# Kernel optimization log

Measured on AMD Instinct MI355X. Metric: run time of the kernel, lower is better.

Reference implementation:

```python
import jax, jax.numpy as jnp
import numpy as np

N_NODES = 50000
N_SCHEMES = 5
K = 16
HIDDEN = 128
N_CLASSES = 8


def setup_inputs() -> dict:
    key = jax.random.key(0)
    ks = jax.random.split(key, 8)
    sc_nei = jax.random.randint(ks[0], (N_SCHEMES, N_NODES, K), 0, N_NODES)
    feats = jax.random.normal(ks[1], (N_NODES, HIDDEN), dtype=jnp.float32)
    W1 = jax.random.normal(ks[2], (HIDDEN, HIDDEN), dtype=jnp.float32) * (1.0 / np.sqrt(HIDDEN))
    b1 = jnp.zeros((HIDDEN,), dtype=jnp.float32)
    W2 = jax.random.normal(ks[3], (HIDDEN, N_CLASSES), dtype=jnp.float32) * (1.0 / np.sqrt(HIDDEN))
    b2 = jnp.zeros((N_CLASSES,), dtype=jnp.float32)
    alpha = jax.random.normal(ks[4], (N_NODES, 1), dtype=jnp.float32)
    attention = jax.random.normal(ks[5], (N_NODES, N_SCHEMES, 1), dtype=jnp.float32)
    return {"sc_nei": sc_nei, "feats": feats, "W1": W1, "b1": b1,
            "W2": W2, "b2": b2, "alpha": alpha, "attention": attention}


def _mlp(x, W1, b1, W2, b2):
    # MLP2 with num_layers=2, dropout in eval mode (identity)
    h = jax.nn.relu(x @ W1 + b1)
    return h @ W2 + b2


def reference(sc_nei, feats, W1, b1, W2, b2, alpha, attention):
    # Per-scheme: gather -> MLP -> exp(log_softmax)=softmax -> mean over neighbors
    emb = feats[sc_nei]                      # [5, N, K, H]
    probs = jax.nn.softmax(_mlp(emb, W1, b1, W2, b2), axis=-1)  # [5, N, K, C]
    sc_cls = probs.mean(axis=2)              # [5, N, C]
    x = jnp.moveaxis(sc_cls, 0, -1)          # [N, C, 5]
    att = jax.nn.softmax(attention, axis=1)  # [N, 5, 1]
    scheme_pred = jnp.squeeze(x @ att, -1)   # [N, C]
    self_pred = jax.nn.softmax(_mlp(feats[:N_NODES], W1, b1, W2, b2), axis=-1)  # [N, C]
    gate = jax.nn.sigmoid(alpha)             # sigmoid(-a) = 1 - sigmoid(a)
    return gate * self_pred + (1.0 - gate) * scheme_pred
```

## Files before the change

### kernel.cpp

```cpp
#include <hip/hip_runtime.h>
#include <math.h>

#define HIDDEN   128
#define NCLS     8
#define NSCHEMES 5
#define KNEI     16

#define MT  64
#define KC  32
#define AS  132
#define WS  136

__global__ __launch_bounds__(256) void mlp_probs(
    const float* __restrict__ feats, const float* __restrict__ W1,
    const float* __restrict__ b1, const float* __restrict__ W2,
    const float* __restrict__ b2, float* __restrict__ probs, int N)
{
    __shared__ float Alds[MT * AS];
    __shared__ float Wc[KC * WS];
    __shared__ float W2lds[HIDDEN * NCLS];
    __shared__ float b1lds[HIDDEN];
    __shared__ float b2lds[NCLS];

    const int tid = threadIdx.x;
    const int nodeBase = blockIdx.x * MT;

    {
        float4 v = ((const float4*)W2)[tid];
        *(float4*)&W2lds[4 * tid] = v;
    }
    if (tid < HIDDEN) b1lds[tid] = b1[tid];
    if (tid < NCLS)   b2lds[tid] = b2[tid];

    #pragma unroll
    for (int idx = tid; idx < MT * HIDDEN / 4; idx += 256) {
        int r = idx >> 5, c4 = idx & 31;
        int n = nodeBase + r; if (n >= N) n = N - 1;
        float4 v = ((const float4*)(feats + (size_t)n * HIDDEN))[c4];
        *(float4*)&Alds[r * AS + 4 * c4] = v;
    }
    __syncthreads();

    const int n0 = tid & 15;
    const int j0 = tid >> 4;

    float acc[4][8];
    #pragma unroll
    for (int r = 0; r < 4; ++r)
        #pragma unroll
        for (int j = 0; j < 8; ++j) acc[r][j] = 0.f;

    for (int kc = 0; kc < HIDDEN; kc += KC) {
        #pragma unroll
        for (int idx = tid; idx < KC * HIDDEN / 4; idx += 256) {
            int i = idx >> 5, c4 = idx & 31;
            float4 v = ((const float4*)(W1 + (size_t)(kc + i) * HIDDEN))[c4];
            *(float4*)&Wc[i * WS + 4 * c4] = v;
        }
        __syncthreads();

        #pragma unroll
        for (int k = 0; k < KC; k += 4) {
            float4 a[4];
            #pragma unroll
            for (int r = 0; r < 4; ++r)
                a[r] = *(const float4*)&Alds[(n0 + 16 * r) * AS + kc + k];
            float4 w[4][2];
            #pragma unroll
            for (int kk = 0; kk < 4; ++kk) {
                w[kk][0] = *(const float4*)&Wc[(k + kk) * WS + 8 * j0];
                w[kk][1] = *(const float4*)&Wc[(k + kk) * WS + 8 * j0 + 4];
            }
            #pragma unroll
            for (int r = 0; r < 4; ++r) {
                float av[4] = {a[r].x, a[r].y, a[r].z, a[r].w};
                #pragma unroll
                for (int kk = 0; kk < 4; ++kk) {
                    acc[r][0] = fmaf(av[kk], w[kk][0].x, acc[r][0]);
                    acc[r][1] = fmaf(av[kk], w[kk][0].y, acc[r][1]);
                    acc[r][2] = fmaf(av[kk], w[kk][0].z, acc[r][2]);
                    acc[r][3] = fmaf(av[kk], w[kk][0].w, acc[r][3]);
                    acc[r][4] = fmaf(av[kk], w[kk][1].x, acc[r][4]);
                    acc[r][5] = fmaf(av[kk], w[kk][1].y, acc[r][5]);
                    acc[r][6] = fmaf(av[kk], w[kk][1].z, acc[r][6]);
                    acc[r][7] = fmaf(av[kk], w[kk][1].w, acc[r][7]);
                }
            }
        }
        __syncthreads();
    }

    #pragma unroll
    for (int r = 0; r < 4; ++r) {
        int row = n0 + 16 * r;
        float4 h0, h1;
        h0.x = fmaxf(acc[r][0] + b1lds[8 * j0 + 0], 0.f);
        h0.y = fmaxf(acc[r][1] + b1lds[8 * j0 + 1], 0.f);
        h0.z = fmaxf(acc[r][2] + b1lds[8 * j0 + 2], 0.f);
        h0.w = fmaxf(acc[r][3] + b1lds[8 * j0 + 3], 0.f);
        h1.x = fmaxf(acc[r][4] + b1lds[8 * j0 + 4], 0.f);
        h1.y = fmaxf(acc[r][5] + b1lds[8 * j0 + 5], 0.f);
        h1.z = fmaxf(acc[r][6] + b1lds[8 * j0 + 6], 0.f);
        h1.w = fmaxf(acc[r][7] + b1lds[8 * j0 + 7], 0.f);
        *(float4*)&Alds[row * AS + 8 * j0]     = h0;
        *(float4*)&Alds[row * AS + 8 * j0 + 4] = h1;
    }
    __syncthreads();

    float (*Opart)[MT][9] = (float (*)[MT][9])Wc;
    {
        const int node = tid & 63;
        const int jr   = tid >> 6;
        float o[NCLS];
        #pragma unroll
        for (int c = 0; c < NCLS; ++c) o[c] = 0.f;
        #pragma unroll
        for (int jj = 0; jj < 32; jj += 4) {
            int j = jr * 32 + jj;
            float4 h = *(const float4*)&Alds[node * AS + j];
            float hv[4] = {h.x, h.y, h.z, h.w};
            #pragma unroll
            for (int q = 0; q < 4; ++q) {
                float4 w0 = *(const float4*)&W2lds[(j + q) * NCLS];
                float4 w1 = *(const float4*)&W2lds[(j + q) * NCLS + 4];
                o[0] = fmaf(hv[q], w0.x, o[0]);
                o[1] = fmaf(hv[q], w0.y, o[1]);
                o[2] = fmaf(hv[q], w0.z, o[2]);
                o[3] = fmaf(hv[q], w0.w, o[3]);
                o[4] = fmaf(hv[q], w1.x, o[4]);
                o[5] = fmaf(hv[q], w1.y, o[5]);
                o[6] = fmaf(hv[q], w1.z, o[6]);
                o[7] = fmaf(hv[q], w1.w, o[7]);
            }
        }
        #pragma unroll
        for (int c = 0; c < NCLS; ++c) Opart[jr][node][c] = o[c];
    }
    __syncthreads();

    if (tid < MT) {
        int n = nodeBase + tid;
        if (n < N) {
            float o[NCLS];
            #pragma unroll
            for (int c = 0; c < NCLS; ++c)
                o[c] = b2lds[c] + Opart[0][tid][c] + Opart[1][tid][c]
                     + Opart[2][tid][c] + Opart[3][tid][c];
            float m = o[0];
            #pragma unroll
            for (int c = 1; c < NCLS; ++c) m = fmaxf(m, o[c]);
            float s = 0.f;
            #pragma unroll
            for (int c = 0; c < NCLS; ++c) { o[c] = __expf(o[c] - m); s += o[c]; }
            float inv = 1.f / s;
            float4* op = (float4*)(probs + (size_t)n * NCLS);
            op[0] = make_float4(o[0] * inv, o[1] * inv, o[2] * inv, o[3] * inv);
            op[1] = make_float4(o[4] * inv, o[5] * inv, o[6] * inv, o[7] * inv);
        }
    }
}

__global__ __launch_bounds__(256) void combine(
    const int* __restrict__ nei, const float* __restrict__ probs,
    const float* __restrict__ attention, const float* __restrict__ alpha,
    float* __restrict__ out, int N)
{
    int t = blockIdx.x * 256 + threadIdx.x;
    int n = t >> 3;
    int c = t & 7;
    if (n >= N) return;

    float aw[NSCHEMES];
    float m = -1e30f;
    #pragma unroll
    for (int s = 0; s < NSCHEMES; ++s) {
        aw[s] = attention[(size_t)n * NSCHEMES + s];
        m = fmaxf(m, aw[s]);
    }
    float ssum = 0.f;
    #pragma unroll
    for (int s = 0; s < NSCHEMES; ++s) { aw[s] = __expf(aw[s] - m); ssum += aw[s]; }
    float invs = 1.f / ssum;

    float acc = 0.f;
    #pragma unroll
    for (int s = 0; s < NSCHEMES; ++s) {
        const int* ip = nei + ((size_t)s * N + n) * KNEI;
        int4 q0 = ((const int4*)ip)[0];
        int4 q1 = ((const int4*)ip)[1];
        int4 q2 = ((const int4*)ip)[2];
        int4 q3 = ((const int4*)ip)[3];
        float p[KNEI];
        p[ 0] = probs[(size_t)q0.x * NCLS + c];
        p[ 1] = probs[(size_t)q0.y * NCLS + c];
        p[ 2] = probs[(size_t)q0.z * NCLS + c];
        p[ 3] = probs[(size_t)q0.w * NCLS + c];
        p[ 4] = probs[(size_t)q1.x * NCLS + c];
        p[ 5] = probs[(size_t)q1.y * NCLS + c];
        p[ 6] = probs[(size_t)q1.z * NCLS + c];
        p[ 7] = probs[(size_t)q1.w * NCLS + c];
        p[ 8] = probs[(size_t)q2.x * NCLS + c];
        p[ 9] = probs[(size_t)q2.y * NCLS + c];
        p[10] = probs[(size_t)q2.z * NCLS + c];
        p[11] = probs[(size_t)q2.w * NCLS + c];
        p[12] = probs[(size_t)q3.x * NCLS + c];
        p[13] = probs[(size_t)q3.y * NCLS + c];
        p[14] = probs[(size_t)q3.z * NCLS + c];
        p[15] = probs[(size_t)q3.w * NCLS + c];
        float sum = ((p[0] + p[1]) + (p[2] + p[3])) + ((p[4] + p[5]) + (p[6] + p[7]))
                  + ((p[8] + p[9]) + (p[10] + p[11])) + ((p[12] + p[13]) + (p[14] + p[15]));
        acc = fmaf(aw[s] * invs * (1.f / (float)KNEI), sum, acc);
    }

    float g = 1.f / (1.f + __expf(-alpha[n]));
    float self = probs[(size_t)n * NCLS + c];
    out[t] = g * self + (1.f - g) * acc;
}

extern "C" void kernel_launch(void* const* d_in, const int* in_sizes, int n_in,
                              void* d_out, int out_size, void* d_ws, size_t ws_size,
                              hipStream_t stream) {
    const int*   sc_nei    = (const int*)d_in[0];
    const float* feats     = (const float*)d_in[1];
    const float* W1        = (const float*)d_in[2];
    const float* b1        = (const float*)d_in[3];
    const float* W2        = (const float*)d_in[4];
    const float* b2        = (const float*)d_in[5];
    const float* alpha     = (const float*)d_in[6];
    const float* attention = (const float*)d_in[7];
    float* out = (float*)d_out;

    int N = in_sizes[1] / HIDDEN;

    float* probs = (float*)d_ws;

    mlp_probs<<<(N + MT - 1) / MT, 256, 0, stream>>>(feats, W1, b1, W2, b2, probs, N);
    combine<<<((N * NCLS) + 255) / 256, 256, 0, stream>>>(sc_nei, probs, attention, alpha, out, N);
}
```

Baseline: 144.9 us.

## Stream feature chunks into small LDS tile and fuse second layer in registers

The full 64x128 feature tile in LDS is replaced by a 64x32 chunk reloaded for each K-chunk. This cuts LDS use per block so more blocks can be resident. The second linear layer is now computed straight from the first-layer accumulators in registers, with partial class sums reduced by cross-lane shuffles and a small LDS reduction across waves. This removes the hidden-activation LDS write/read and a barrier, but adds per-chunk feature loads, extra register pressure from the o[4][8] array, and shuffles.

```diff
diff --git a/kernel.cpp b/kernel.cpp
--- a/kernel.cpp
+++ b/kernel.cpp
@@ -6,43 +6,33 @@
 #define NSCHEMES 5
 #define KNEI     16
 
-#define MT  64
-#define KC  32
-#define AS  132
-#define WS  136
+#define MT   64
+#define KC   32
+#define ASTR 36
+#define WSTR 136
 
 __global__ __launch_bounds__(256) void mlp_probs(
     const float* __restrict__ feats, const float* __restrict__ W1,
     const float* __restrict__ b1, const float* __restrict__ W2,
     const float* __restrict__ b2, float* __restrict__ probs, int N)
 {
-    __shared__ float Alds[MT * AS];
-    __shared__ float Wc[KC * WS];
+    __shared__ float Ach[MT * ASTR];
+    __shared__ float Wc[KC * WSTR];
     __shared__ float W2lds[HIDDEN * NCLS];
-    __shared__ float b1lds[HIDDEN];
-    __shared__ float b2lds[NCLS];
+    __shared__ float b1v[HIDDEN];
+    __shared__ float b2v[NCLS];
 
     const int tid = threadIdx.x;
     const int nodeBase = blockIdx.x * MT;
+    const int n0 = tid & 15;
+    const int j0 = tid >> 4;
 
     {
         float4 v = ((const float4*)W2)[tid];
         *(float4*)&W2lds[4 * tid] = v;
     }
-    if (tid < HIDDEN) b1lds[tid] = b1[tid];
-    if (tid < NCLS)   b2lds[tid] = b2[tid];
-
-    #pragma unroll
-    for (int idx = tid; idx < MT * HIDDEN / 4; idx += 256) {
-        int r = idx >> 5, c4 = idx & 31;
-        int n = nodeBase + r; if (n >= N) n = N - 1;
-        float4 v = ((const float4*)(feats + (size_t)n * HIDDEN))[c4];
-        *(float4*)&Alds[r * AS + 4 * c4] = v;
-    }
-    __syncthreads();
-
-    const int n0 = tid & 15;
-    const int j0 = tid >> 4;
+    if (tid < HIDDEN) b1v[tid] = b1[tid];
+    if (tid < NCLS)   b2v[tid] = b2[tid];
 
     float acc[4][8];
     #pragma unroll
@@ -51,11 +41,18 @@
         for (int j = 0; j < 8; ++j) acc[r][j] = 0.f;
 
     for (int kc = 0; kc < HIDDEN; kc += KC) {
+        #pragma unroll
+        for (int idx = tid; idx < MT * KC / 4; idx += 256) {
+            int r = idx >> 3, c4 = idx & 7;
+            int n = nodeBase + r; if (n >= N) n = N - 1;
+            float4 v = ((const float4*)(feats + (size_t)n * HIDDEN + kc))[c4];
+            *(float4*)&Ach[r * ASTR + 4 * c4] = v;
+        }
         #pragma unroll
         for (int idx = tid; idx < KC * HIDDEN / 4; idx += 256) {
             int i = idx >> 5, c4 = idx & 31;
             float4 v = ((const float4*)(W1 + (size_t)(kc + i) * HIDDEN))[c4];
-            *(float4*)&Wc[i * WS + 4 * c4] = v;
+            *(float4*)&Wc[i * WSTR + 4 * c4] = v;
         }
         __syncthreads();
 
@@ -64,12 +61,12 @@
             float4 a[4];
             #pragma unroll
             for (int r = 0; r < 4; ++r)
-                a[r] = *(const float4*)&Alds[(n0 + 16 * r) * AS + kc + k];
+                a[r] = *(const float4*)&Ach[(n0 + 16 * r) * ASTR + k];
             float4 w[4][2];
             #pragma unroll
             for (int kk = 0; kk < 4; ++kk) {
-                w[kk][0] = *(const float4*)&Wc[(k + kk) * WS + 8 * j0];
-                w[kk][1] = *(const float4*)&Wc[(k + kk) * WS + 8 * j0 + 4];
+                w[kk][0] = *(const float4*)&Wc[(k + kk) * WSTR + 8 * j0];
+                w[kk][1] = *(const float4*)&Wc[(k + kk) * WSTR + 8 * j0 + 4];
             }
             #pragma unroll
             for (int r = 0; r < 4; ++r) {
@@ -90,72 +87,87 @@
         __syncthreads();
     }
 
-    #pragma unroll
-    for (int r = 0; r < 4; ++r) {
-        int row = n0 + 16 * r;
-        float4 h0, h1;
-        h0.x = fmaxf(acc[r][0] + b1lds[8 * j0 + 0], 0.f);
-        h0.y = fmaxf(acc[r][1] + b1lds[8 * j0 + 1], 0.f);
-        h0.z = fmaxf(acc[r][2] + b1lds[8 * j0 + 2], 0.f);
-        h0.w = fmaxf(acc[r][3] + b1lds[8 * j0 + 3], 0.f);
-        h1.x = fmaxf(acc[r][4] + b1lds[8 * j0 + 4], 0.f);
-        h1.y = fmaxf(acc[r][5] + b1lds[8 * j0 + 5], 0.f);
-        h1.z = fmaxf(acc[r][6] + b1lds[8 * j0 + 6], 0.f);
-        h1.w = fmaxf(acc[r][7] + b1lds[8 * j0 + 7], 0.f);
-        *(float4*)&Alds[row * AS + 8 * j0]     = h0;
-        *(float4*)&Alds[row * AS + 8 * j0 + 4] = h1;
-    }
-    __syncthreads();
-
-    float (*Opart)[MT][9] = (float (*)[MT][9])Wc;
     {
-        const int node = tid & 63;
-        const int jr   = tid >> 6;
-        float o[NCLS];
-        #pragma unroll
-        for (int c = 0; c < NCLS; ++c) o[c] = 0.f;
-        #pragma unroll
-        for (int jj = 0; jj < 32; jj += 4) {
-            int j = jr * 32 + jj;
-            float4 h = *(const float4*)&Alds[node * AS + j];
-            float hv[4] = {h.x, h.y, h.z, h.w};
-            #pragma unroll
-            for (int q = 0; q < 4; ++q) {
-                float4 w0 = *(const float4*)&W2lds[(j + q) * NCLS];
-                float4 w1 = *(const float4*)&W2lds[(j + q) * NCLS + 4];
-                o[0] = fmaf(hv[q], w0.x, o[0]);
-                o[1] = fmaf(hv[q], w0.y, o[1]);
-                o[2] = fmaf(hv[q], w0.z, o[2]);
-                o[3] = fmaf(hv[q], w0.w, o[3]);
-                o[4] = fmaf(hv[q], w1.x, o[4]);
-                o[5] = fmaf(hv[q], w1.y, o[5]);
-                o[6] = fmaf(hv[q], w1.z, o[6]);
-                o[7] = fmaf(hv[q], w1.w, o[7]);
-            }
-        }
-        #pragma unroll
-        for (int c = 0; c < NCLS; ++c) Opart[jr][node][c] = o[c];
+        float4 bA = *(const float4*)&b1v[8 * j0];
+        float4 bB = *(const float4*)&b1v[8 * j0 + 4];
+        float bb[8] = {bA.x, bA.y, bA.z, bA.w, bB.x, bB.y, bB.z, bB.w};
+        #pragma unroll
+        for (int r = 0; r < 4; ++r)
+            #pragma unroll
+            for (int j = 0; j < 8; ++j)
+                acc[r][j] = fmaxf(acc[r][j] + bb[j], 0.f);
+    }
+
+    float o[4][NCLS];
+    #pragma unroll
+    for (int r = 0; r < 4; ++r)
+        #pragma unroll
+        for (int c = 0; c < NCLS; ++c) o[r][c] = 0.f;
+
+    #pragma unroll
+    for (int jj = 0; jj < 8; ++jj) {
+        float4 w0 = *(const float4*)&W2lds[(8 * j0 + jj) * NCLS];
+        float4 w1 = *(const float4*)&W2lds[(8 * j0 + jj) * NCLS + 4];
+        #pragma unroll
+        for (int r = 0; r < 4; ++r) {
+            float h = acc[r][jj];
+            o[r][0] = fmaf(h, w0.x, o[r][0]);
+            o[r][1] = fmaf(h, w0.y, o[r][1]);
+            o[r][2] = fmaf(h, w0.z, o[r][2]);
+            o[r][3] = fmaf(h, w0.w, o[r][3]);
+            o[r][4] = fmaf(h, w1.x, o[r][4]);
+            o[r][5] = fmaf(h, w1.y, o[r][5]);
+            o[r][6] = fmaf(h, w1.z, o[r][6]);
+            o[r][7] = fmaf(h, w1.w, o[r][7]);
+        }
+    }
+
+    #pragma unroll
+    for (int r = 0; r < 4; ++r)
+        #pragma unroll
+        for (int c = 0; c < NCLS; ++c) {
+            float v = o[r][c];
+            v += __shfl_xor(v, 16, 64);
+            v += __shfl_xor(v, 32, 64);
+            o[r][c] = v;
+        }
+
+    float* Red = Wc;
+    const int wv = tid >> 6;
+    if ((tid & 48) == 0) {
+        #pragma unroll
+        for (int r = 0; r < 4; ++r) {
+            int node = n0 + 16 * r;
+            float* dst = &Red[(wv * MT + node) * 12];
+            *(float4*)dst       = make_float4(o[r][0], o[r][1], o[r][2], o[r][3]);
+            *(float4*)(dst + 4) = make_float4(o[r][4], o[r][5], o[r][6], o[r][7]);
+        }
     }
     __syncthreads();
 
     if (tid < MT) {
         int n = nodeBase + tid;
         if (n < N) {
-            float o[NCLS];
-            #pragma unroll
-            for (int c = 0; c < NCLS; ++c)
-                o[c] = b2lds[c] + Opart[0][tid][c] + Opart[1][tid][c]
-                     + Opart[2][tid][c] + Opart[3][tid][c];
-            float m = o[0];
-            #pragma unroll
-            for (int c = 1; c < NCLS; ++c) m = fmaxf(m, o[c]);
+            float oo[NCLS];
+            #pragma unroll
+            for (int c = 0; c < NCLS; ++c) oo[c] = b2v[c];
+            #pragma unroll
+            for (int w = 0; w < 4; ++w) {
+                float4 p0 = *(const float4*)&Red[(w * MT + tid) * 12];
+                float4 p1 = *(const float4*)&Red[(w * MT + tid) * 12 + 4];
+                oo[0] += p0.x; oo[1] += p0.y; oo[2] += p0.z; oo[3] += p0.w;
+                oo[4] += p1.x; oo[5] += p1.y; oo[6] += p1.z; oo[7] += p1.w;
+            }
+            float m = oo[0];
+            #pragma unroll
+            for (int c = 1; c < NCLS; ++c) m = fmaxf(m, oo[c]);
             float s = 0.f;
             #pragma unroll
-            for (int c = 0; c < NCLS; ++c) { o[c] = __expf(o[c] - m); s += o[c]; }
+            for (int c = 0; c < NCLS; ++c) { oo[c] = __expf(oo[c] - m); s += oo[c]; }
             float inv = 1.f / s;
             float4* op = (float4*)(probs + (size_t)n * NCLS);
-            op[0] = make_float4(o[0] * inv, o[1] * inv, o[2] * inv, o[3] * inv);
-            op[1] = make_float4(o[4] * inv, o[5] * inv, o[6] * inv, o[7] * inv);
+            op[0] = make_float4(oo[0] * inv, oo[1] * inv, oo[2] * inv, oo[3] * inv);
+            op[1] = make_float4(oo[4] * inv, oo[5] * inv, oo[6] * inv, oo[7] * inv);
         }
     }
 }
```

Measured after the change: 141.1 us. 2.6% less time.
